# Performance work log

Hardware: AMD Instinct MI355X
Metric: run time of the kernel (lower is better)

## Reference

```python
import jax, jax.numpy as jnp
import numpy as np

D = 256
H = 4
HD = D // H


def rotate_half(x):
    xp = x.reshape(x.shape[:-1] + (-1, 2))
    x1, x2 = xp[..., 0], xp[..., 1]
    return jnp.stack((-x2, x1), axis=-1).reshape(x.shape)


def apply_rope(freqs, t):
    # freqs: [2, B, 1, N, HD]; t: [B, H, N, HD]
    return t * freqs[0] + rotate_half(t) * freqs[1]


def layernorm(x, g, b, eps=1e-5):
    m = jnp.mean(x, axis=-1, keepdims=True)
    v = jnp.var(x, axis=-1, keepdims=True)
    return (x - m) * jax.lax.rsqrt(v + eps) * g + b


def ffn(z, W1, b1, g, be, W2, b2):
    h = layernorm(z @ W1 + b1, g, be)
    h = jax.nn.gelu(h, approximate=False)
    return h @ W2 + b2


def heads_split(t):
    B, N, _ = t.shape
    return t.reshape(B, N, H, HD).transpose(0, 2, 1, 3)  # [B,H,N,HD]


def heads_merge(t):
    B, h, N, hd = t.shape
    return t.transpose(0, 2, 1, 3).reshape(B, N, h * hd)


def sdpa(q, k, v):
    s = q.shape[-1] ** (-0.5)
    sim = jnp.einsum('bhid,bhjd->bhij', q, k) * s
    attn = jax.nn.softmax(sim, axis=-1)
    return jnp.einsum('bhij,bhjd->bhid', attn, v)


def self_block(x, enc, Wqkv, bqkv, Wo, bo, W1, b1, g, be, W2, b2):
    B, N, _ = x.shape
    qkv = (x @ Wqkv + bqkv).reshape(B, N, H, HD, 3).transpose(0, 2, 1, 3, 4)
    q, k, v = qkv[..., 0], qkv[..., 1], qkv[..., 2]
    q = apply_rope(enc, q)
    k = apply_rope(enc, k)
    msg = heads_merge(sdpa(q, k, v)) @ Wo + bo
    return x + ffn(jnp.concatenate([x, msg], axis=-1), W1, b1, g, be, W2, b2)


def cross_block(x0, x1, Wqk, bqk, Wv, bv, Wo, bo, W1, b1, g, be, W2, b2):
    qk0 = heads_split(x0 @ Wqk + bqk)
    qk1 = heads_split(x1 @ Wqk + bqk)
    v0 = heads_split(x0 @ Wv + bv)
    v1 = heads_split(x1 @ Wv + bv)
    s = HD ** (-0.5)
    qk0 = qk0 * (s ** 0.5)
    qk1 = qk1 * (s ** 0.5)
    sim = jnp.einsum('bhid,bhjd->bhij', qk0, qk1)
    attn01 = jax.nn.softmax(sim, axis=-1)
    attn10 = jax.nn.softmax(sim.transpose(0, 1, 3, 2), axis=-1)
    m0 = jnp.einsum('bhij,bhjd->bhid', attn01, v1)
    m1 = jnp.einsum('bhij,bhjd->bhid', attn10, v0)
    m0 = heads_merge(m0) @ Wo + bo
    m1 = heads_merge(m1) @ Wo + bo
    x0 = x0 + ffn(jnp.concatenate([x0, m0], axis=-1), W1, b1, g, be, W2, b2)
    x1 = x1 + ffn(jnp.concatenate([x1, m1], axis=-1), W1, b1, g, be, W2, b2)
    return x0, x1


def setup_inputs() -> dict:
    key = jax.random.key(0)
    ks = jax.random.split(key, 24)
    B, N = 4, 2048
    desc0 = jax.random.normal(ks[0], (B, N, D), jnp.float32)
    desc1 = jax.random.normal(ks[1], (B, N, D), jnp.float32)
    encoding0 = jax.random.uniform(ks[2], (2, B, 1, N, HD), jnp.float32)
    encoding1 = jax.random.uniform(ks[3], (2, B, 1, N, HD), jnp.float32)

    def lin(k, fin, fout):
        k1, k2 = jax.random.split(k)
        W = jax.random.normal(k1, (fin, fout), jnp.float32) * (fin ** -0.5)
        b = jax.random.normal(k2, (fout,), jnp.float32) * 0.01
        return W, b

    Wqkv, bqkv = lin(ks[4], D, 3 * D)
    Wo_s, bo_s = lin(ks[5], D, D)
    W1_s, b1_s = lin(ks[6], 2 * D, 2 * D)
    g_s = jnp.ones((2 * D,), jnp.float32)
    be_s = jnp.zeros((2 * D,), jnp.float32)
    W2_s, b2_s = lin(ks[7], 2 * D, D)
    Wqk_c, bqk_c = lin(ks[8], D, D)
    Wv_c, bv_c = lin(ks[9], D, D)
    Wo_c, bo_c = lin(ks[10], D, D)
    W1_c, b1_c = lin(ks[11], 2 * D, 2 * D)
    g_c = jnp.ones((2 * D,), jnp.float32)
    be_c = jnp.zeros((2 * D,), jnp.float32)
    W2_c, b2_c = lin(ks[12], 2 * D, D)
    return dict(desc0=desc0, desc1=desc1, encoding0=encoding0, encoding1=encoding1,
                Wqkv=Wqkv, bqkv=bqkv, Wo_s=Wo_s, bo_s=bo_s,
                W1_s=W1_s, b1_s=b1_s, g_s=g_s, be_s=be_s, W2_s=W2_s, b2_s=b2_s,
                Wqk_c=Wqk_c, bqk_c=bqk_c, Wv_c=Wv_c, bv_c=bv_c, Wo_c=Wo_c, bo_c=bo_c,
                W1_c=W1_c, b1_c=b1_c, g_c=g_c, be_c=be_c, W2_c=W2_c, b2_c=b2_c)


def reference(desc0, desc1, encoding0, encoding1,
              Wqkv, bqkv, Wo_s, bo_s, W1_s, b1_s, g_s, be_s, W2_s, b2_s,
              Wqk_c, bqk_c, Wv_c, bv_c, Wo_c, bo_c, W1_c, b1_c, g_c, be_c, W2_c, b2_c):
    d0 = self_block(desc0, encoding0, Wqkv, bqkv, Wo_s, bo_s, W1_s, b1_s, g_s, be_s, W2_s, b2_s)
    d1 = self_block(desc1, encoding1, Wqkv, bqkv, Wo_s, bo_s, W1_s, b1_s, g_s, be_s, W2_s, b2_s)
    return cross_block(d0, d1, Wqk_c, bqk_c, Wv_c, bv_c, Wo_c, bo_c, W1_c, b1_c, g_c, be_c, W2_c, b2_c)
```

## Files before the change

### kernel.cpp

```cpp
#include <hip/hip_runtime.h>
#include <math.h>

#define BB 4
#define HH 4
#define NN 2048
#define DD 256
#define HDIM 64
#define NTOK 8192
#define NTOK2 16384

typedef __attribute__((ext_vector_type(8))) __bf16 bf16x8;
typedef __attribute__((ext_vector_type(8))) unsigned short ushort8;
typedef __attribute__((ext_vector_type(4))) float floatx4;
typedef __attribute__((ext_vector_type(4))) short short4v;

union U8 { ushort8 u; bf16x8 b; };
union U4 { unsigned int u[2]; unsigned long long l; short4v s; };

#define MFMA16(a, b, c) __builtin_amdgcn_mfma_f32_16x16x16bf16_1k(a, b, c, 0, 0, 0)

__device__ __forceinline__ unsigned short f2bf(float x) {
    unsigned int u = __float_as_uint(x);
    u += 0x7FFF + ((u >> 16) & 1);
    return (unsigned short)(u >> 16);
}
__device__ __forceinline__ float bf2f(unsigned short u) {
    return __uint_as_float(((unsigned int)u) << 16);
}
__device__ __forceinline__ unsigned int pkbf(float a, float b) {
    return ((__float_as_uint(a) + 0x8000u) >> 16) |
           ((__float_as_uint(b) + 0x8000u) & 0xFFFF0000u);
}

struct WTab {
    const float* w[7];
    unsigned short* o[7];
    int K[7];
    int N[7];
    int st[7];
    int t0[8];
};

__global__ __launch_bounds__(256) void wtrans(WTab tab)
{
    __shared__ float lds[32][33];
    const int t = threadIdx.x;
    int bid = blockIdx.x;
    int s = 0;
    while (bid >= tab.t0[s + 1]) s++;
    const int ti = bid - tab.t0[s];
    const int K = tab.K[s], N = tab.N[s], st = tab.st[s];
    const int tx = ti % (N / 32), ty = ti / (N / 32);
    const int k0 = ty * 32, n0 = tx * 32;
    const float* W = tab.w[s];
    unsigned short* Wt = tab.o[s];

    {
        int r = t >> 3, c = (t & 7) * 4;
        float4 a = *(const float4*)&W[(size_t)(k0 + r) * N + n0 + c];
        lds[r][c] = a.x; lds[r][c+1] = a.y; lds[r][c+2] = a.z; lds[r][c+3] = a.w;
    }
    __syncthreads();
    {
        int n = t >> 3, kq = (t & 7) * 4;
        ushort4 p;
        p.x = f2bf(lds[kq+0][n]); p.y = f2bf(lds[kq+1][n]);
        p.z = f2bf(lds[kq+2][n]); p.w = f2bf(lds[kq+3][n]);
        *(ushort4*)&Wt[(size_t)(n0 + n) * st + k0 + kq] = p;
    }
}

__global__ __launch_bounds__(256) void wfuse(
    const float* __restrict__ Wo_s, const float* __restrict__ W1_s,
    unsigned short* __restrict__ o_s,
    const float* __restrict__ Wo_c, const float* __restrict__ W1_c,
    unsigned short* __restrict__ o_c)
{
    __shared__ float wo[32][33];
    __shared__ float w1[32][68];
    const int t = threadIdx.x;
    const int bid = blockIdx.x;
    const int seg = bid >> 6, ti_ = bid & 63;
    const int i0 = (ti_ >> 3) * 32, n0 = (ti_ & 7) * 64;
    const float* Wo  = seg ? Wo_c : Wo_s;
    const float* W1b = (seg ? W1_c : W1_s) + 256 * 512;
    unsigned short* out = seg ? o_c : o_s;
    const int ti = t >> 3, tn = t & 7;

    float acc[8] = {};
    for (int jc = 0; jc < 256; jc += 32) {
        {
            int r = t >> 3, c = (t & 7) * 4;
            *(float4*)&wo[r][c] = *(const float4*)&Wo[(size_t)(i0 + r) * 256 + jc + c];
            int c8 = (t & 7) * 8;
            *(float4*)&w1[r][c8]     = *(const float4*)&W1b[(size_t)(jc + r) * 512 + n0 + c8];
            *(float4*)&w1[r][c8 + 4] = *(const float4*)&W1b[(size_t)(jc + r) * 512 + n0 + c8 + 4];
        }
        __syncthreads();
        #pragma unroll
        for (int j = 0; j < 32; j++) {
            float a = wo[ti][j];
            #pragma unroll
            for (int e = 0; e < 8; e++) acc[e] += a * w1[j][tn * 8 + e];
        }
        __syncthreads();
    }
    #pragma unroll
    for (int e = 0; e < 8; e++)
        out[(size_t)(n0 + tn * 8 + e) * 512 + 256 + i0 + ti] = f2bf(acc[e]);
}

__global__ __launch_bounds__(256) void bfuse(
    const float* bo_s, const float* W1_s, const float* b1_s, float* bs,
    const float* bo_c, const float* W1_c, const float* b1_c, float* bc)
{
    const int seg = blockIdx.x >> 1, half = blockIdx.x & 1;
    const int n = half * 256 + threadIdx.x;
    const float* bo  = seg ? bo_c : bo_s;
    const float* W1b = (seg ? W1_c : W1_s) + 256 * 512;
    const float* b1  = seg ? b1_c : b1_s;
    float* out       = seg ? bc : bs;
    float a = b1[n];
    for (int j = 0; j < 256; j++) a += bo[j] * W1b[(size_t)j * 512 + n];
    out[n] = a;
}

__global__ __launch_bounds__(256) void gemm_mfma(
    const unsigned short* __restrict__ A, int lda,
    const unsigned short* __restrict__ Wt, int K,
    const float* __restrict__ bias, const float* __restrict__ bias2, int mode,
    float* outF, unsigned short* outH0, unsigned short* outH1,
    unsigned short* outH2,
    int ldc, const float* R0, const float* R1)
{
    __shared__ __align__(16) unsigned short As[64 * 40];
    __shared__ __align__(16) unsigned short Bs[128 * 40];
    const int t = threadIdx.x;
    const int w = t >> 6, lane = t & 63, quad = lane >> 4, l15 = lane & 15;
    const int m0 = blockIdx.y * 64, n0 = blockIdx.x * 128;
    const int wn = w * 32;
    const int sar = t >> 2, sac = (t & 3) * 8;
    const int sbr = t >> 1, sbc = (t & 1) * 16;

    const unsigned short* Ap = A  + (size_t)(m0 + sar) * lda + sac;
    const unsigned short* Bp = Wt + (size_t)(n0 + sbr) * K   + sbc;

    ushort8 pa  = *(const ushort8*)(Ap);
    ushort8 pb0 = *(const ushort8*)(Bp);
    ushort8 pb1 = *(const ushort8*)(Bp + 8);

    floatx4 acc[4][2];
    #pragma unroll
    for (int i = 0; i < 4; i++)
        #pragma unroll
        for (int j = 0; j < 2; j++) acc[i][j] = (floatx4){0.f, 0.f, 0.f, 0.f};

    const int nk = K >> 5;
    for (int kk = 0; kk < nk; kk++) {
        *(ushort8*)&As[sar * 40 + sac]     = pa;
        *(ushort8*)&Bs[sbr * 40 + sbc]     = pb0;
        *(ushort8*)&Bs[sbr * 40 + sbc + 8] = pb1;
        __syncthreads();
        if (kk + 1 < nk) {
            int ko = (kk + 1) * 32;
            pa  = *(const ushort8*)(Ap + ko);
            pb0 = *(const ushort8*)(Bp + ko);
            pb1 = *(const ushort8*)(Bp + ko + 8);
        }
        U8 af[4], bf[2];
        #pragma unroll
        for (int i = 0; i < 4; i++)
            af[i].u = *(const ushort8*)&As[(i * 16 + l15) * 40 + quad * 8];
        #pragma unroll
        for (int j = 0; j < 2; j++)
            bf[j].u = *(const ushort8*)&Bs[(wn + j * 16 + l15) * 40 + quad * 8];
        #pragma unroll
        for (int i = 0; i < 4; i++)
            #pragma unroll
            for (int j = 0; j < 2; j++)
                acc[i][j] = __builtin_amdgcn_mfma_f32_16x16x32_bf16(af[i].b, bf[j].b, acc[i][j], 0, 0, 0);
        __syncthreads();
    }

    #pragma unroll
    for (int i = 0; i < 4; i++) {
        #pragma unroll
        for (int j = 0; j < 2; j++) {
            int col = n0 + wn + j * 16 + l15;
            float bv = (mode == 2 && col >= 256) ? bias2[col & 255] : bias[col];
            #pragma unroll
            for (int r = 0; r < 4; r++) {
                int grow = m0 + i * 16 + quad * 4 + r;
                float v = acc[i][j][r] + bv;
                if (mode == 1) {
                    outH0[(size_t)grow * ldc + col] = f2bf(v);
                } else if (mode == 2) {
                    int cc = col & 255;
                    int h = cc >> 6, d = cc & 63;
                    int ds = grow >> 13, b = (grow >> 11) & 3, n = grow & 2047;
                    int bh = ds * 16 + b * 4 + h;
                    if (col < 256)
                        outH0[((size_t)bh * NN + n) * HDIM + d] = f2bf(v);
                    else
                        outH1[((size_t)bh * HDIM + d) * NN + n] = f2bf(v);
                } else if (mode == 3) {
                    int sel = col % 3, cc = col / 3;
                    int h = cc >> 6, d = cc & 63;
                    int ds = grow >> 13, b = (grow >> 11) & 3, n = grow & 2047;
                    int bh = ds * 16 + b * 4 + h;
                    if (sel == 0)
                        outH0[((size_t)bh * NN + n) * HDIM + d] = f2bf(v);
                    else if (sel == 1)
                        outH1[((size_t)bh * NN + n) * HDIM + d] = f2bf(v);
                    else
                        outH2[((size_t)bh * HDIM + d) * NN + n] = f2bf(v);
                } else {
                    const float* R = (grow < NTOK) ? R0 : R1;
                    float vv = v + R[(size_t)(grow & 8191) * 256 + col];
                    outF[(size_t)grow * 256 + col] = vv;
                    if (outH0) outH0[(size_t)grow * 256 + col] = f2bf(vv);
                    if (outH1) outH1[(size_t)grow * 512 + col] = f2bf(vv);
                }
            }
        }
    }
}

__global__ __launch_bounds__(256) void rope_k(unsigned short* __restrict__ qb,
                                              unsigned short* __restrict__ kb,
                                              const float* __restrict__ enc0,
                                              const float* __restrict__ enc1)
{
    int i = blockIdx.x * 256 + threadIdx.x;
    int dp = (i & 31) * 2;
    int n  = (i >> 5) & (NN - 1);
    int h  = (i >> 16) & 3;
    int b  = (i >> 18) & 3;
    int ds = (i >> 20) & 1;
    int bf = (i >> 21) & 1;
    unsigned short* tq = (bf ? kb : qb) +
        (((size_t)(ds * 16 + b * 4 + h)) * NN + n) * HDIM + dp;
    const float* e0 = (ds ? enc1 : enc0) + ((size_t)b * NN + n) * HDIM + dp;
    const float* e1 = e0 + (size_t)BB * NN * HDIM;
    float x0 = bf2f(tq[0]), x1 = bf2f(tq[1]);
    float y0 = x0 * e0[0] - x1 * e1[0];
    float y1 = x1 * e0[1] + x0 * e1[1];
    tq[0] = f2bf(y0); tq[1] = f2bf(y1);
}

__global__ __launch_bounds__(256) void flash_attn(
    const unsigned short* __restrict__ Q, const unsigned short* __restrict__ K,
    const unsigned short* __restrict__ V, unsigned short* __restrict__ O,
    int ldo, int kvx, float qscale)
{
    __shared__ __align__(16) unsigned short Ks[64 * 72];
    __shared__ __align__(16) unsigned short Vt[64 * 72];

    const int t    = threadIdx.x;
    const int w    = t >> 6;
    const int lane = t & 63;
    const int quad = lane >> 4;
    const int l15  = lane & 15;
    const int bh   = blockIdx.y;
    const int kbh  = bh ^ kvx;
    const int q0   = blockIdx.x * 64;

    const unsigned short* Qb  = Q + (size_t)bh  * NN * HDIM;
    const unsigned short* Kb  = K + (size_t)kbh * NN * HDIM;
    const unsigned short* VTb = V + (size_t)kbh * NN * HDIM;

    const int srf = t >> 3, scf = (t & 7) * 8;

    const int qrow = q0 + w * 16 + l15;
    bf16x8 qf0, qf1;
    {
        U8 r0, r1, x0, x1;
        r0.u = *(const ushort8*)&Qb[(size_t)qrow * HDIM + quad * 8];
        r1.u = *(const ushort8*)&Qb[(size_t)qrow * HDIM + 32 + quad * 8];
        #pragma unroll
        for (int j = 0; j < 8; j++) {
            x0.u[j] = f2bf(bf2f(r0.u[j]) * qscale);
            x1.u[j] = f2bf(bf2f(r1.u[j]) * qscale);
        }
        qf0 = x0.b; qf1 = x1.b;
    }

    floatx4 o[4];
    #pragma unroll
    for (int c = 0; c < 4; c++) o[c] = (floatx4){0.f, 0.f, 0.f, 0.f};
    float m = -1e30f, l = 0.f;

    ushort8 ka0 = *(const ushort8*)&Kb[(size_t)srf * HDIM + scf];
    ushort8 ka1 = *(const ushort8*)&Kb[(size_t)(srf + 32) * HDIM + scf];
    ushort8 va0 = *(const ushort8*)&VTb[(size_t)srf * NN + scf];
    ushort8 va1 = *(const ushort8*)&VTb[(size_t)(srf + 32) * NN + scf];

    for (int j0 = 0; j0 < NN; j0 += 64) {
        *(ushort8*)&Ks[srf * 72 + scf]        = ka0;
        *(ushort8*)&Ks[(srf + 32) * 72 + scf] = ka1;
        *(ushort8*)&Vt[srf * 72 + scf]        = va0;
        *(ushort8*)&Vt[(srf + 32) * 72 + scf] = va1;
        __syncthreads();
        if (j0 + 64 < NN) {
            int jn = j0 + 64;
            ka0 = *(const ushort8*)&Kb[(size_t)(jn + srf) * HDIM + scf];
            ka1 = *(const ushort8*)&Kb[(size_t)(jn + srf + 32) * HDIM + scf];
            va0 = *(const ushort8*)&VTb[(size_t)srf * NN + jn + scf];
            va1 = *(const ushort8*)&VTb[(size_t)(srf + 32) * NN + jn + scf];
        }

        floatx4 s[4];
        #pragma unroll
        for (int t4 = 0; t4 < 4; t4++) {
            U8 k0, k1;
            k0.u = *(const ushort8*)&Ks[(t4 * 16 + l15) * 72 + quad * 8];
            k1.u = *(const ushort8*)&Ks[(t4 * 16 + l15) * 72 + 32 + quad * 8];
            floatx4 z = (floatx4){0.f, 0.f, 0.f, 0.f};
            z = __builtin_amdgcn_mfma_f32_16x16x32_bf16(k0.b, qf0, z, 0, 0, 0);
            z = __builtin_amdgcn_mfma_f32_16x16x32_bf16(k1.b, qf1, z, 0, 0, 0);
            s[t4] = z;
        }

        float mx = s[0][0];
        #pragma unroll
        for (int t4 = 0; t4 < 4; t4++)
            #pragma unroll
            for (int r = 0; r < 4; r++) mx = fmaxf(mx, s[t4][r]);
        mx = fmaxf(mx, __shfl_xor(mx, 16, 64));
        mx = fmaxf(mx, __shfl_xor(mx, 32, 64));
        float mn = fmaxf(m, mx);
        float al = exp2f(m - mn);
        m = mn;
        float rs = 0.f;
        #pragma unroll
        for (int t4 = 0; t4 < 4; t4++)
            #pragma unroll
            for (int r = 0; r < 4; r++) {
                float p = exp2f(s[t4][r] - mn);
                s[t4][r] = p;
                rs += p;
            }
        rs += __shfl_xor(rs, 16, 64);
        rs += __shfl_xor(rs, 32, 64);
        l = l * al + rs;
        #pragma unroll
        for (int c = 0; c < 4; c++)
            #pragma unroll
            for (int r = 0; r < 4; r++) o[c][r] *= al;

        short4v pf[4];
        #pragma unroll
        for (int t4 = 0; t4 < 4; t4++) {
            U4 pk;
            pk.u[0] = pkbf(s[t4][0], s[t4][1]);
            pk.u[1] = pkbf(s[t4][2], s[t4][3]);
            pf[t4] = pk.s;
        }

        #pragma unroll
        for (int c = 0; c < 4; c++) {
            #pragma unroll
            for (int t4 = 0; t4 < 4; t4++) {
                U4 vf;
                vf.l = *(const unsigned long long*)
                    &Vt[(c * 16 + l15) * 72 + t4 * 16 + quad * 4];
                o[c] = MFMA16(vf.s, pf[t4], o[c]);
            }
        }
        __syncthreads();
    }

    const int ds = bh >> 4, b = (bh >> 2) & 3, h = bh & 3;
    const int q = q0 + w * 16 + l15;
    const size_t row = (size_t)ds * NTOK + b * NN + q;
    float inv = 1.f / l;
    #pragma unroll
    for (int c = 0; c < 4; c++) {
        ushort4 pk;
        pk.x = f2bf(o[c][0] * inv);
        pk.y = f2bf(o[c][1] * inv);
        pk.z = f2bf(o[c][2] * inv);
        pk.w = f2bf(o[c][3] * inv);
        *(ushort4*)&O[row * ldo + h * HDIM + c * 16 + quad * 4] = pk;
    }
}

__global__ __launch_bounds__(256) void ln_gelu(
    unsigned short* __restrict__ hb, const float* __restrict__ g,
    const float* __restrict__ be)
{
    __shared__ float r1[4], r2[4];
    const int t = threadIdx.x;
    const size_t row = blockIdx.x;
    unsigned short* ip = hb + row * 512;
    float x0 = bf2f(ip[t]), x1 = bf2f(ip[t + 256]);
    float s = x0 + x1, ss = x0 * x0 + x1 * x1;
    #pragma unroll
    for (int o = 32; o > 0; o >>= 1) { s += __shfl_down(s, o); ss += __shfl_down(ss, o); }
    if ((t & 63) == 0) { r1[t >> 6] = s; r2[t >> 6] = ss; }
    __syncthreads();
    float S  = r1[0] + r1[1] + r1[2] + r1[3];
    float SS = r2[0] + r2[1] + r2[2] + r2[3];
    float mean = S * (1.f / 512.f);
    float var  = SS * (1.f / 512.f) - mean * mean;
    float inv  = rsqrtf(var + 1e-5f);
    float y0 = (x0 - mean) * inv * g[t]       + be[t];
    float y1 = (x1 - mean) * inv * g[t + 256] + be[t + 256];
    ip[t]       = f2bf(0.5f * y0 * (1.f + erff(y0 * 0.70710678f)));
    ip[t + 256] = f2bf(0.5f * y1 * (1.f + erff(y1 * 0.70710678f)));
}

__global__ __launch_bounds__(256) void copy_to_cat(
    const float* __restrict__ s0, const float* __restrict__ s1,
    unsigned short* __restrict__ cat)
{
    int i = blockIdx.x * 256 + threadIdx.x;
    int row = i >> 6, c4 = (i & 63) * 4;
    const float* s = (row < NTOK) ? s0 : s1;
    float4 a = *(const float4*)&s[(size_t)(row & 8191) * 256 + c4];
    ushort4 p = { f2bf(a.x), f2bf(a.y), f2bf(a.z), f2bf(a.w) };
    *(ushort4*)&cat[(size_t)row * 512 + c4] = p;
}

extern "C" void kernel_launch(void* const* d_in, const int* in_sizes, int n_in,
                              void* d_out, int out_size, void* d_ws, size_t ws_size,
                              hipStream_t stream)
{
    const float* desc0 = (const float*)d_in[0];
    const float* desc1 = (const float*)d_in[1];
    const float* enc0  = (const float*)d_in[2];
    const float* enc1  = (const float*)d_in[3];
    const float* Wqkv  = (const float*)d_in[4];  const float* bqkv  = (const float*)d_in[5];
    const float* Wo_s  = (const float*)d_in[6];  const float* bo_s  = (const float*)d_in[7];
    const float* W1_s  = (const float*)d_in[8];  const float* b1_s  = (const float*)d_in[9];
    const float* g_s   = (const float*)d_in[10]; const float* be_s  = (const float*)d_in[11];
    const float* W2_s  = (const float*)d_in[12]; const float* b2_s  = (const float*)d_in[13];
    const float* Wqk_c = (const float*)d_in[14]; const float* bqk_c = (const float*)d_in[15];
    const float* Wv_c  = (const float*)d_in[16]; const float* bv_c  = (const float*)d_in[17];
    const float* Wo_c  = (const float*)d_in[18]; const float* bo_c  = (const float*)d_in[19];
    const float* W1_c  = (const float*)d_in[20]; const float* b1_c  = (const float*)d_in[21];
    const float* g_c   = (const float*)d_in[22]; const float* be_c  = (const float*)d_in[23];
    const float* W2_c  = (const float*)d_in[24]; const float* b2_c  = (const float*)d_in[25];

    char* ws = (char*)d_ws;
    unsigned short* wt  = (unsigned short*)ws;
    unsigned short* qb  = (unsigned short*)(ws + 2490368);
    unsigned short* kb  = (unsigned short*)(ws + 10878976);
    unsigned short* vb  = (unsigned short*)(ws + 27656192);
    unsigned short* cat = (unsigned short*)(ws + 36044800);
    unsigned short* hb  = (unsigned short*)(ws + 52822016);
    unsigned short* dbf = (unsigned short*)(ws + 86376448);

    unsigned short* t_qkv  = wt;
    float*          bias_s = (float*)(wt + 196608);
    unsigned short* t_w1s  = wt + 262144;
    unsigned short* t_w2s  = wt + 524288;
    unsigned short* t_wqkc = wt + 655360;
    float*          bias_c = (float*)(wt + 786432);
    unsigned short* t_w1c  = wt + 851968;
    unsigned short* t_w2c  = wt + 1114112;

    float* outF = (float*)d_out;

    dim3 blk(256);

    WTab tab;
    tab.w[0] = Wqkv;  tab.o[0] = t_qkv;          tab.K[0] = 256; tab.N[0] = 768; tab.st[0] = 256;
    tab.w[1] = W1_s;  tab.o[1] = t_w1s;          tab.K[1] = 256; tab.N[1] = 512; tab.st[1] = 512;
    tab.w[2] = W2_s;  tab.o[2] = t_w2s;          tab.K[2] = 512; tab.N[2] = 256; tab.st[2] = 512;
    tab.w[3] = Wqk_c; tab.o[3] = t_wqkc;         tab.K[3] = 256; tab.N[3] = 256; tab.st[3] = 256;
    tab.w[4] = Wv_c;  tab.o[4] = t_wqkc + 65536; tab.K[4] = 256; tab.N[4] = 256; tab.st[4] = 256;
    tab.w[5] = W1_c;  tab.o[5] = t_w1c;          tab.K[5] = 256; tab.N[5] = 512; tab.st[5] = 512;
    tab.w[6] = W2_c;  tab.o[6] = t_w2c;          tab.K[6] = 512; tab.N[6] = 256; tab.st[6] = 512;
    int acc_t = 0;
    for (int s = 0; s < 7; s++) {
        tab.t0[s] = acc_t;
        acc_t += (tab.K[s] / 32) * (tab.N[s] / 32);
    }
    tab.t0[7] = acc_t;
    hipLaunchKernelGGL(wtrans, dim3(acc_t), blk, 0, stream, tab);
    hipLaunchKernelGGL(wfuse, dim3(128), blk, 0, stream,
                       Wo_s, W1_s, t_w1s, Wo_c, W1_c, t_w1c);
    hipLaunchKernelGGL(bfuse, dim3(4), blk, 0, stream,
                       bo_s, W1_s, b1_s, bias_s, bo_c, W1_c, b1_c, bias_c);

    auto gemm = [&](const unsigned short* A, int lda, const unsigned short* Wtp,
                    int K, const float* bias, const float* bias2, int Nc, int mode,
                    float* oF, unsigned short* oh0, unsigned short* oh1,
                    unsigned short* oh2, int ldc, const float* r0, const float* r1) {
        dim3 g(Nc / 128, NTOK2 / 64);
        hipLaunchKernelGGL(gemm_mfma, g, blk, 0, stream,
                           A, lda, Wtp, K, bias, bias2, mode,
                           oF, oh0, oh1, oh2, ldc, r0, r1);
    };

    const float QS = 0.125f * 1.44269504088896f;

    hipLaunchKernelGGL(copy_to_cat, dim3(4096), blk, 0, stream, desc0, desc1, cat);
    gemm(cat, 512, t_qkv, 256, bqkv, nullptr, 768, 3,
         nullptr, qb, kb, vb, 0, nullptr, nullptr);
    hipLaunchKernelGGL(rope_k, dim3(16384), blk, 0, stream, qb, kb, enc0, enc1);
    hipLaunchKernelGGL(flash_attn, dim3(NN / 64, 32), blk, 0, stream,
                       qb, kb, vb, cat + 256, 512, 0, QS);
    gemm(cat, 512, t_w1s, 512, bias_s, nullptr, 512, 1,
         nullptr, hb, nullptr, nullptr, 512, nullptr, nullptr);
    hipLaunchKernelGGL(ln_gelu, dim3(NTOK2), blk, 0, stream, hb, g_s, be_s);
    gemm(hb, 512, t_w2s, 512, b2_s, nullptr, 256, 4,
         outF, dbf, cat, nullptr, 256, desc0, desc1);

    gemm(dbf, 256, t_wqkc, 256, bqk_c, bv_c, 512, 2,
         nullptr, qb, vb, nullptr, 0, nullptr, nullptr);
    hipLaunchKernelGGL(flash_attn, dim3(NN / 64, 32), blk, 0, stream,
                       qb, qb, vb, cat + 256, 512, 16, QS);
    gemm(cat, 512, t_w1c, 512, bias_c, nullptr, 512, 1,
         nullptr, hb, nullptr, nullptr, 512, nullptr, nullptr);
    hipLaunchKernelGGL(ln_gelu, dim3(NTOK2), blk, 0, stream, hb, g_c, be_c);
    gemm(hb, 512, t_w2c, 512, b2_c, nullptr, 256, 4,
         outF, nullptr, nullptr, nullptr, 256, outF, outF + (size_t)NTOK * 256);
}
```

Measured before the change: 494.2 us.

## Enlarge GEMM tiles to 128x128, double flash-attention KV tile, skip redundant rescale

The projection GEMMs move to a 128x128 block tile with a 2x2 warp layout, so each warp computes a 64x64 sub-tile and operands get more reuse from shared memory. The W2 residual GEMM is split into its own specialized kernel that keeps the old 64x128 tile. Flash attention now stages 128 keys per iteration instead of 64, halving the number of barrier and softmax rounds. It also skips the running max/sum rescale when no lane's max increased. The larger tiles raise register and LDS use, which may lower occupancy, and the GEMMs launch fewer blocks.

```diff
diff --git a/kernel.cpp b/kernel.cpp
--- a/kernel.cpp
+++ b/kernel.cpp
@@ -125,59 +125,60 @@
     out[n] = a;
 }
 
-__global__ __launch_bounds__(256) void gemm_mfma(
+__global__ __launch_bounds__(256) void gemm128(
     const unsigned short* __restrict__ A, int lda,
     const unsigned short* __restrict__ Wt, int K,
     const float* __restrict__ bias, const float* __restrict__ bias2, int mode,
-    float* outF, unsigned short* outH0, unsigned short* outH1,
-    unsigned short* outH2,
-    int ldc, const float* R0, const float* R1)
-{
-    __shared__ __align__(16) unsigned short As[64 * 40];
+    unsigned short* outH0, unsigned short* outH1, unsigned short* outH2,
+    int ldc)
+{
+    __shared__ __align__(16) unsigned short As[128 * 40];
     __shared__ __align__(16) unsigned short Bs[128 * 40];
     const int t = threadIdx.x;
     const int w = t >> 6, lane = t & 63, quad = lane >> 4, l15 = lane & 15;
-    const int m0 = blockIdx.y * 64, n0 = blockIdx.x * 128;
-    const int wn = w * 32;
-    const int sar = t >> 2, sac = (t & 3) * 8;
-    const int sbr = t >> 1, sbc = (t & 1) * 16;
-
-    const unsigned short* Ap = A  + (size_t)(m0 + sar) * lda + sac;
-    const unsigned short* Bp = Wt + (size_t)(n0 + sbr) * K   + sbc;
-
-    ushort8 pa  = *(const ushort8*)(Ap);
+    const int m0 = blockIdx.y * 128, n0 = blockIdx.x * 128;
+    const int wm = (w >> 1) * 64, wn = (w & 1) * 64;
+    const int sr = t >> 1, sc = (t & 1) * 16;
+
+    const unsigned short* Ap = A  + (size_t)(m0 + sr) * lda + sc;
+    const unsigned short* Bp = Wt + (size_t)(n0 + sr) * K   + sc;
+
+    ushort8 pa0 = *(const ushort8*)(Ap);
+    ushort8 pa1 = *(const ushort8*)(Ap + 8);
     ushort8 pb0 = *(const ushort8*)(Bp);
     ushort8 pb1 = *(const ushort8*)(Bp + 8);
 
-    floatx4 acc[4][2];
+    floatx4 acc[4][4];
     #pragma unroll
     for (int i = 0; i < 4; i++)
         #pragma unroll
-        for (int j = 0; j < 2; j++) acc[i][j] = (floatx4){0.f, 0.f, 0.f, 0.f};
+        for (int j = 0; j < 4; j++) acc[i][j] = (floatx4){0.f, 0.f, 0.f, 0.f};
 
     const int nk = K >> 5;
     for (int kk = 0; kk < nk; kk++) {
-        *(ushort8*)&As[sar * 40 + sac]     = pa;
-        *(ushort8*)&Bs[sbr * 40 + sbc]     = pb0;
-        *(ushort8*)&Bs[sbr * 40 + sbc + 8] = pb1;
+        *(ushort8*)&As[sr * 40 + sc]     = pa0;
+        *(ushort8*)&As[sr * 40 + sc + 8] = pa1;
+        *(ushort8*)&Bs[sr * 40 + sc]     = pb0;
+        *(ushort8*)&Bs[sr * 40 + sc + 8] = pb1;
         __syncthreads();
         if (kk + 1 < nk) {
             int ko = (kk + 1) * 32;
-            pa  = *(const ushort8*)(Ap + ko);
+            pa0 = *(const ushort8*)(Ap + ko);
+            pa1 = *(const ushort8*)(Ap + ko + 8);
             pb0 = *(const ushort8*)(Bp + ko);
             pb1 = *(const ushort8*)(Bp + ko + 8);
         }
-        U8 af[4], bf[2];
+        U8 af[4], bf[4];
         #pragma unroll
         for (int i = 0; i < 4; i++)
-            af[i].u = *(const ushort8*)&As[(i * 16 + l15) * 40 + quad * 8];
-        #pragma unroll
-        for (int j = 0; j < 2; j++)
+            af[i].u = *(const ushort8*)&As[(wm + i * 16 + l15) * 40 + quad * 8];
+        #pragma unroll
+        for (int j = 0; j < 4; j++)
             bf[j].u = *(const ushort8*)&Bs[(wn + j * 16 + l15) * 40 + quad * 8];
         #pragma unroll
         for (int i = 0; i < 4; i++)
             #pragma unroll
-            for (int j = 0; j < 2; j++)
+            for (int j = 0; j < 4; j++)
                 acc[i][j] = __builtin_amdgcn_mfma_f32_16x16x32_bf16(af[i].b, bf[j].b, acc[i][j], 0, 0, 0);
         __syncthreads();
     }
@@ -185,12 +186,12 @@
     #pragma unroll
     for (int i = 0; i < 4; i++) {
         #pragma unroll
-        for (int j = 0; j < 2; j++) {
+        for (int j = 0; j < 4; j++) {
             int col = n0 + wn + j * 16 + l15;
             float bv = (mode == 2 && col >= 256) ? bias2[col & 255] : bias[col];
             #pragma unroll
             for (int r = 0; r < 4; r++) {
-                int grow = m0 + i * 16 + quad * 4 + r;
+                int grow = m0 + wm + i * 16 + quad * 4 + r;
                 float v = acc[i][j][r] + bv;
                 if (mode == 1) {
                     outH0[(size_t)grow * ldc + col] = f2bf(v);
@@ -203,7 +204,7 @@
                         outH0[((size_t)bh * NN + n) * HDIM + d] = f2bf(v);
                     else
                         outH1[((size_t)bh * HDIM + d) * NN + n] = f2bf(v);
-                } else if (mode == 3) {
+                } else {
                     int sel = col % 3, cc = col / 3;
                     int h = cc >> 6, d = cc & 63;
                     int ds = grow >> 13, b = (grow >> 11) & 3, n = grow & 2047;
@@ -214,13 +215,83 @@
                         outH1[((size_t)bh * NN + n) * HDIM + d] = f2bf(v);
                     else
                         outH2[((size_t)bh * HDIM + d) * NN + n] = f2bf(v);
-                } else {
-                    const float* R = (grow < NTOK) ? R0 : R1;
-                    float vv = v + R[(size_t)(grow & 8191) * 256 + col];
-                    outF[(size_t)grow * 256 + col] = vv;
-                    if (outH0) outH0[(size_t)grow * 256 + col] = f2bf(vv);
-                    if (outH1) outH1[(size_t)grow * 512 + col] = f2bf(vv);
                 }
+            }
+        }
+    }
+}
+
+__global__ __launch_bounds__(256) void gemm_w2(
+    const unsigned short* __restrict__ A,
+    const unsigned short* __restrict__ Wt,
+    const float* __restrict__ bias,
+    float* outF, unsigned short* outH0, unsigned short* outH1,
+    const float* R0, const float* R1)
+{
+    __shared__ __align__(16) unsigned short As[64 * 40];
+    __shared__ __align__(16) unsigned short Bs[128 * 40];
+    const int t = threadIdx.x;
+    const int w = t >> 6, lane = t & 63, quad = lane >> 4, l15 = lane & 15;
+    const int m0 = blockIdx.y * 64, n0 = blockIdx.x * 128;
+    const int wn = w * 32;
+    const int sar = t >> 2, sac = (t & 3) * 8;
+    const int sbr = t >> 1, sbc = (t & 1) * 16;
+    const int K = 512;
+
+    const unsigned short* Ap = A  + (size_t)(m0 + sar) * 512 + sac;
+    const unsigned short* Bp = Wt + (size_t)(n0 + sbr) * K   + sbc;
+
+    ushort8 pa  = *(const ushort8*)(Ap);
+    ushort8 pb0 = *(const ushort8*)(Bp);
+    ushort8 pb1 = *(const ushort8*)(Bp + 8);
+
+    floatx4 acc[4][2];
+    #pragma unroll
+    for (int i = 0; i < 4; i++)
+        #pragma unroll
+        for (int j = 0; j < 2; j++) acc[i][j] = (floatx4){0.f, 0.f, 0.f, 0.f};
+
+    const int nk = K >> 5;
+    for (int kk = 0; kk < nk; kk++) {
+        *(ushort8*)&As[sar * 40 + sac]     = pa;
+        *(ushort8*)&Bs[sbr * 40 + sbc]     = pb0;
+        *(ushort8*)&Bs[sbr * 40 + sbc + 8] = pb1;
+        __syncthreads();
+        if (kk + 1 < nk) {
+            int ko = (kk + 1) * 32;
+            pa  = *(const ushort8*)(Ap + ko);
+            pb0 = *(const ushort8*)(Bp + ko);
+            pb1 = *(const ushort8*)(Bp + ko + 8);
+        }
+        U8 af[4], bf[2];
+        #pragma unroll
+        for (int i = 0; i < 4; i++)
+            af[i].u = *(const ushort8*)&As[(i * 16 + l15) * 40 + quad * 8];
+        #pragma unroll
+        for (int j = 0; j < 2; j++)
+            bf[j].u = *(const ushort8*)&Bs[(wn + j * 16 + l15) * 40 + quad * 8];
+        #pragma unroll
+        for (int i = 0; i < 4; i++)
+            #pragma unroll
+            for (int j = 0; j < 2; j++)
+                acc[i][j] = __builtin_amdgcn_mfma_f32_16x16x32_bf16(af[i].b, bf[j].b, acc[i][j], 0, 0, 0);
+        __syncthreads();
+    }
+
+    #pragma unroll
+    for (int i = 0; i < 4; i++) {
+        #pragma unroll
+        for (int j = 0; j < 2; j++) {
+            int col = n0 + wn + j * 16 + l15;
+            float bv = bias[col];
+            #pragma unroll
+            for (int r = 0; r < 4; r++) {
+                int grow = m0 + i * 16 + quad * 4 + r;
+                const float* R = (grow < NTOK) ? R0 : R1;
+                float vv = acc[i][j][r] + bv + R[(size_t)(grow & 8191) * 256 + col];
+                outF[(size_t)grow * 256 + col] = vv;
+                if (outH0) outH0[(size_t)grow * 256 + col] = f2bf(vv);
+                if (outH1) outH1[(size_t)grow * 512 + col] = f2bf(vv);
             }
         }
     }
@@ -253,8 +324,8 @@
     const unsigned short* __restrict__ V, unsigned short* __restrict__ O,
     int ldo, int kvx, float qscale)
 {
-    __shared__ __align__(16) unsigned short Ks[64 * 72];
-    __shared__ __align__(16) unsigned short Vt[64 * 72];
+    __shared__ __align__(16) unsigned short Ks[128 * 72];
+    __shared__ __align__(16) unsigned short Vt[64 * 136];
 
     const int t    = threadIdx.x;
     const int w    = t >> 6;
@@ -269,7 +340,8 @@
     const unsigned short* Kb  = K + (size_t)kbh * NN * HDIM;
     const unsigned short* VTb = V + (size_t)kbh * NN * HDIM;
 
-    const int srf = t >> 3, scf = (t & 7) * 8;
+    const int krf = t >> 3, kcf = (t & 7) * 8;
+    const int vrf = t >> 4, vcf = (t & 15) * 8;
 
     const int qrow = q0 + w * 16 + l15;
     bf16x8 qf0, qf1;
@@ -290,81 +362,88 @@
     for (int c = 0; c < 4; c++) o[c] = (floatx4){0.f, 0.f, 0.f, 0.f};
     float m = -1e30f, l = 0.f;
 
-    ushort8 ka0 = *(const ushort8*)&Kb[(size_t)srf * HDIM + scf];
-    ushort8 ka1 = *(const ushort8*)&Kb[(size_t)(srf + 32) * HDIM + scf];
-    ushort8 va0 = *(const ushort8*)&VTb[(size_t)srf * NN + scf];
-    ushort8 va1 = *(const ushort8*)&VTb[(size_t)(srf + 32) * NN + scf];
-
-    for (int j0 = 0; j0 < NN; j0 += 64) {
-        *(ushort8*)&Ks[srf * 72 + scf]        = ka0;
-        *(ushort8*)&Ks[(srf + 32) * 72 + scf] = ka1;
-        *(ushort8*)&Vt[srf * 72 + scf]        = va0;
-        *(ushort8*)&Vt[(srf + 32) * 72 + scf] = va1;
-        __syncthreads();
-        if (j0 + 64 < NN) {
-            int jn = j0 + 64;
-            ka0 = *(const ushort8*)&Kb[(size_t)(jn + srf) * HDIM + scf];
-            ka1 = *(const ushort8*)&Kb[(size_t)(jn + srf + 32) * HDIM + scf];
-            va0 = *(const ushort8*)&VTb[(size_t)srf * NN + jn + scf];
-            va1 = *(const ushort8*)&VTb[(size_t)(srf + 32) * NN + jn + scf];
-        }
-
-        floatx4 s[4];
-        #pragma unroll
-        for (int t4 = 0; t4 < 4; t4++) {
+    ushort8 ka[4], va[4];
+    #pragma unroll
+    for (int i = 0; i < 4; i++) {
+        ka[i] = *(const ushort8*)&Kb[(size_t)(krf + 32 * i) * HDIM + kcf];
+        va[i] = *(const ushort8*)&VTb[(size_t)(vrf + 16 * i) * NN + vcf];
+    }
+
+    for (int j0 = 0; j0 < NN; j0 += 128) {
+        #pragma unroll
+        for (int i = 0; i < 4; i++) {
+            *(ushort8*)&Ks[(krf + 32 * i) * 72 + kcf]  = ka[i];
+            *(ushort8*)&Vt[(vrf + 16 * i) * 136 + vcf] = va[i];
+        }
+        __syncthreads();
+        if (j0 + 128 < NN) {
+            int jn = j0 + 128;
+            #pragma unroll
+            for (int i = 0; i < 4; i++) {
+                ka[i] = *(const ushort8*)&Kb[(size_t)(jn + krf + 32 * i) * HDIM + kcf];
+                va[i] = *(const ushort8*)&VTb[(size_t)(vrf + 16 * i) * NN + jn + vcf];
+            }
+        }
+
+        floatx4 s[8];
+        #pragma unroll
+        for (int t8 = 0; t8 < 8; t8++) {
             U8 k0, k1;
-            k0.u = *(const ushort8*)&Ks[(t4 * 16 + l15) * 72 + quad * 8];
-            k1.u = *(const ushort8*)&Ks[(t4 * 16 + l15) * 72 + 32 + quad * 8];
+            k0.u = *(const ushort8*)&Ks[(t8 * 16 + l15) * 72 + quad * 8];
+            k1.u = *(const ushort8*)&Ks[(t8 * 16 + l15) * 72 + 32 + quad * 8];
             floatx4 z = (floatx4){0.f, 0.f, 0.f, 0.f};
             z = __builtin_amdgcn_mfma_f32_16x16x32_bf16(k0.b, qf0, z, 0, 0, 0);
             z = __builtin_amdgcn_mfma_f32_16x16x32_bf16(k1.b, qf1, z, 0, 0, 0);
-            s[t4] = z;
+            s[t8] = z;
         }
 
         float mx = s[0][0];
         #pragma unroll
-        for (int t4 = 0; t4 < 4; t4++)
-            #pragma unroll
-            for (int r = 0; r < 4; r++) mx = fmaxf(mx, s[t4][r]);
+        for (int t8 = 0; t8 < 8; t8++)
+            #pragma unroll
+            for (int r = 0; r < 4; r++) mx = fmaxf(mx, s[t8][r]);
         mx = fmaxf(mx, __shfl_xor(mx, 16, 64));
         mx = fmaxf(mx, __shfl_xor(mx, 32, 64));
-        float mn = fmaxf(m, mx);
-        float al = exp2f(m - mn);
-        m = mn;
+        if (__ballot(mx > m)) {
+            float mn = fmaxf(m, mx);
+            float al = exp2f(m - mn);
+            m = mn;
+            l *= al;
+            #pragma unroll
+            for (int c = 0; c < 4; c++)
+                #pragma unroll
+                for (int r = 0; r < 4; r++) o[c][r] *= al;
+        }
         float rs = 0.f;
         #pragma unroll
-        for (int t4 = 0; t4 < 4; t4++)
+        for (int t8 = 0; t8 < 8; t8++)
             #pragma unroll
             for (int r = 0; r < 4; r++) {
-                float p = exp2f(s[t4][r] - mn);
-                s[t4][r] = p;
+                float p = exp2f(s[t8][r] - m);
+                s[t8][r] = p;
                 rs += p;
             }
         rs += __shfl_xor(rs, 16, 64);
         rs += __shfl_xor(rs, 32, 64);
-        l = l * al + rs;
-        #pragma unroll
-        for (int c = 0; c < 4; c++)
-            #pragma unroll
-            for (int r = 0; r < 4; r++) o[c][r] *= al;
-
-        short4v pf[4];
-        #pragma unroll
-        for (int t4 = 0; t4 < 4; t4++) {
+        l += rs;
+
+        short4v pf[8];
+        #pragma unroll
+        for (int t8 = 0; t8 < 8; t8++) {
             U4 pk;
-            pk.u[0] = pkbf(s[t4][0], s[t4][1]);
-            pk.u[1] = pkbf(s[t4][2], s[t4][3]);
-            pf[t4] = pk.s;
+            pk.u[0] = pkbf(s[t8][0], s[t8][1]);
+            pk.u[1] = pkbf(s[t8][2], s[t8][3]);
+            pf[t8] = pk.s;
         }
 
         #pragma unroll
         for (int c = 0; c < 4; c++) {
             #pragma unroll
-            for (int t4 = 0; t4 < 4; t4++) {
+            for (int t8 = 0; t8 < 8; t8++) {
                 U4 vf;
                 vf.l = *(const unsigned long long*)
-                    &Vt[(c * 16 + l15) * 72 + t4 * 16 + quad * 4];
-                o[c] = MFMA16(vf.s, pf[t4], o[c]);
+                    &Vt[(c * 16 + l15) * 136 + t8 * 16 + quad * 4];
+                o[c] = MFMA16(vf.s, pf[t8], o[c]);
             }
         }
         __syncthreads();
@@ -484,37 +563,33 @@
     hipLaunchKernelGGL(bfuse, dim3(4), blk, 0, stream,
                        bo_s, W1_s, b1_s, bias_s, bo_c, W1_c, b1_c, bias_c);
 
-    auto gemm = [&](const unsigned short* A, int lda, const unsigned short* Wtp,
+    auto g128 = [&](const unsigned short* A, int lda, const unsigned short* Wtp,
                     int K, const float* bias, const float* bias2, int Nc, int mode,
-                    float* oF, unsigned short* oh0, unsigned short* oh1,
-                    unsigned short* oh2, int ldc, const float* r0, const float* r1) {
-        dim3 g(Nc / 128, NTOK2 / 64);
-        hipLaunchKernelGGL(gemm_mfma, g, blk, 0, stream,
-                           A, lda, Wtp, K, bias, bias2, mode,
-                           oF, oh0, oh1, oh2, ldc, r0, r1);
+                    unsigned short* oh0, unsigned short* oh1, unsigned short* oh2,
+                    int ldc) {
+        dim3 g(Nc / 128, NTOK2 / 128);
+        hipLaunchKernelGGL(gemm128, g, blk, 0, stream,
+                           A, lda, Wtp, K, bias, bias2, mode, oh0, oh1, oh2, ldc);
     };
 
     const float QS = 0.125f * 1.44269504088896f;
 
     hipLaunchKernelGGL(copy_to_cat, dim3(4096), blk, 0, stream, desc0, desc1, cat);
-    gemm(cat, 512, t_qkv, 256, bqkv, nullptr, 768, 3,
-         nullptr, qb, kb, vb, 0, nullptr, nullptr);
+    g128(cat, 512, t_qkv, 256, bqkv, nullptr, 768, 3, qb, kb, vb, 0);
     hipLaunchKernelGGL(rope_k, dim3(16384), blk, 0, stream, qb, kb, enc0, enc1);
     hipLaunchKernelGGL(flash_attn, dim3(NN / 64, 32), blk, 0, stream,
                        qb, kb, vb, cat + 256, 512, 0, QS);
-    gemm(cat, 512, t_w1s, 512, bias_s, nullptr, 512, 1,
-         nullptr, hb, nullptr, nullptr, 512, nullptr, nullptr);
+    g128(cat, 512, t_w1s, 512, bias_s, nullptr, 512, 1, hb, nullptr, nullptr, 512);
     hipLaunchKernelGGL(ln_gelu, dim3(NTOK2), blk, 0, stream, hb, g_s, be_s);
-    gemm(hb, 512, t_w2s, 512, b2_s, nullptr, 256, 4,
-         outF, dbf, cat, nullptr, 256, desc0, desc1);
-
-    gemm(dbf, 256, t_wqkc, 256, bqk_c, bv_c, 512, 2,
-         nullptr, qb, vb, nullptr, 0, nullptr, nullptr);
+    hipLaunchKernelGGL(gemm_w2, dim3(2, 256), blk, 0, stream,
+                       hb, t_w2s, b2_s, outF, dbf, cat, desc0, desc1);
+
+    g128(dbf, 256, t_wqkc, 256, bqk_c, bv_c, 512, 2, qb, vb, nullptr, 0);
     hipLaunchKernelGGL(flash_attn, dim3(NN / 64, 32), blk, 0, stream,
                        qb, qb, vb, cat + 256, 512, 16, QS);
-    gemm(cat, 512, t_w1c, 512, bias_c, nullptr, 512, 1,
-         nullptr, hb, nullptr, nullptr, 512, nullptr, nullptr);
+    g128(cat, 512, t_w1c, 512, bias_c, nullptr, 512, 1, hb, nullptr, nullptr, 512);
     hipLaunchKernelGGL(ln_gelu, dim3(NTOK2), blk, 0, stream, hb, g_c, be_c);
-    gemm(hb, 512, t_w2c, 512, b2_c, nullptr, 256, 4,
-         outF, nullptr, nullptr, nullptr, 256, outF, outF + (size_t)NTOK * 256);
-}
+    hipLaunchKernelGGL(gemm_w2, dim3(2, 256), blk, 0, stream,
+                       hb, t_w2c, b2_c, outF, nullptr, nullptr,
+                       outF, outF + (size_t)NTOK * 256);
+}
```

New measurement: 497.6 us. Within noise of the previous version (+0.7%).

## Fuse input cast into QKV GEMM and Q-rope plus desc copy into attention

Applied to the files above, without the earlier changes.

The QKV GEMM now reads the fp32 descriptors directly and converts them to bf16 while loading, so the separate copy_to_cat kernel is removed. The flash attention kernel applies RoPE to Q in registers when it loads Q. It also writes the bf16 copy of the descriptors into the left half of the concat buffer. The rope kernel now only processes K, halving its launch. This removes launches and round trips through global memory, at the cost of a runtime branch in the GEMM A-load and extra strided fp32 encoding reads in attention.

```diff
diff --git a/kernel.cpp b/kernel.cpp
--- a/kernel.cpp
+++ b/kernel.cpp
@@ -126,7 +126,7 @@
 }
 
 __global__ __launch_bounds__(256) void gemm_mfma(
-    const unsigned short* __restrict__ A, int lda,
+    const void* A0v, const void* A1v, int lda, int a_f32,
     const unsigned short* __restrict__ Wt, int K,
     const float* __restrict__ bias, const float* __restrict__ bias2, int mode,
     float* outF, unsigned short* outH0, unsigned short* outH1,
@@ -141,11 +141,26 @@
     const int wn = w * 32;
     const int sar = t >> 2, sac = (t & 3) * 8;
     const int sbr = t >> 1, sbc = (t & 1) * 16;
-
-    const unsigned short* Ap = A  + (size_t)(m0 + sar) * lda + sac;
-    const unsigned short* Bp = Wt + (size_t)(n0 + sbr) * K   + sbc;
-
-    ushort8 pa  = *(const ushort8*)(Ap);
+    const int mside = (m0 >= 8192) ? 1 : 0;
+    const int mrow = m0 & 8191;
+    const unsigned short* Ah = (const unsigned short*)(mside ? A1v : A0v);
+    const float* Af = (const float*)(mside ? A1v : A0v);
+
+    const unsigned short* Bp = Wt + (size_t)(n0 + sbr) * K + sbc;
+
+    auto loadA = [&](int ko) -> ushort8 {
+        if (a_f32) {
+            float4 x = *(const float4*)&Af[(size_t)(mrow + sar) * lda + ko + sac];
+            float4 y = *(const float4*)&Af[(size_t)(mrow + sar) * lda + ko + sac + 4];
+            ushort8 r;
+            r[0] = f2bf(x.x); r[1] = f2bf(x.y); r[2] = f2bf(x.z); r[3] = f2bf(x.w);
+            r[4] = f2bf(y.x); r[5] = f2bf(y.y); r[6] = f2bf(y.z); r[7] = f2bf(y.w);
+            return r;
+        }
+        return *(const ushort8*)&Ah[(size_t)(mrow + sar) * lda + ko + sac];
+    };
+
+    ushort8 pa  = loadA(0);
     ushort8 pb0 = *(const ushort8*)(Bp);
     ushort8 pb1 = *(const ushort8*)(Bp + 8);
 
@@ -163,7 +178,7 @@
         __syncthreads();
         if (kk + 1 < nk) {
             int ko = (kk + 1) * 32;
-            pa  = *(const ushort8*)(Ap + ko);
+            pa  = loadA(ko);
             pb0 = *(const ushort8*)(Bp + ko);
             pb1 = *(const ushort8*)(Bp + ko + 8);
         }
@@ -226,8 +241,7 @@
     }
 }
 
-__global__ __launch_bounds__(256) void rope_k(unsigned short* __restrict__ qb,
-                                              unsigned short* __restrict__ kb,
+__global__ __launch_bounds__(256) void rope_k(unsigned short* __restrict__ kb,
                                               const float* __restrict__ enc0,
                                               const float* __restrict__ enc1)
 {
@@ -237,8 +251,7 @@
     int h  = (i >> 16) & 3;
     int b  = (i >> 18) & 3;
     int ds = (i >> 20) & 1;
-    int bf = (i >> 21) & 1;
-    unsigned short* tq = (bf ? kb : qb) +
+    unsigned short* tq = kb +
         (((size_t)(ds * 16 + b * 4 + h)) * NN + n) * HDIM + dp;
     const float* e0 = (ds ? enc1 : enc0) + ((size_t)b * NN + n) * HDIM + dp;
     const float* e1 = e0 + (size_t)BB * NN * HDIM;
@@ -251,7 +264,9 @@
 __global__ __launch_bounds__(256) void flash_attn(
     const unsigned short* __restrict__ Q, const unsigned short* __restrict__ K,
     const unsigned short* __restrict__ V, unsigned short* __restrict__ O,
-    int ldo, int kvx, float qscale)
+    int ldo, int kvx, float qscale,
+    const float* __restrict__ e0g, const float* __restrict__ e1g,
+    const float* __restrict__ d0, const float* __restrict__ d1)
 {
     __shared__ __align__(16) unsigned short Ks[64 * 72];
     __shared__ __align__(16) unsigned short Vt[64 * 72];
@@ -264,6 +279,7 @@
     const int bh   = blockIdx.y;
     const int kbh  = bh ^ kvx;
     const int q0   = blockIdx.x * 64;
+    const int ds   = bh >> 4, b = (bh >> 2) & 3, h = bh & 3;
 
     const unsigned short* Qb  = Q + (size_t)bh  * NN * HDIM;
     const unsigned short* Kb  = K + (size_t)kbh * NN * HDIM;
@@ -277,10 +293,31 @@
         U8 r0, r1, x0, x1;
         r0.u = *(const ushort8*)&Qb[(size_t)qrow * HDIM + quad * 8];
         r1.u = *(const ushort8*)&Qb[(size_t)qrow * HDIM + 32 + quad * 8];
+        float xa[8], xb[8];
+        #pragma unroll
+        for (int j = 0; j < 8; j++) { xa[j] = bf2f(r0.u[j]); xb[j] = bf2f(r1.u[j]); }
+        if (e0g) {
+            const float* eb = ds ? e1g : e0g;
+            size_t base = ((size_t)(b * NN + qrow)) * HDIM;
+            const float* f0a = eb + base + quad * 8;
+            const float* f1a = f0a + (size_t)BB * NN * HDIM;
+            const float* f0b = eb + base + 32 + quad * 8;
+            const float* f1b = f0b + (size_t)BB * NN * HDIM;
+            float ya[8], yb[8];
+            #pragma unroll
+            for (int p = 0; p < 4; p++) {
+                ya[2*p]   = xa[2*p]   * f0a[2*p]   - xa[2*p+1] * f1a[2*p];
+                ya[2*p+1] = xa[2*p+1] * f0a[2*p+1] + xa[2*p]   * f1a[2*p+1];
+                yb[2*p]   = xb[2*p]   * f0b[2*p]   - xb[2*p+1] * f1b[2*p];
+                yb[2*p+1] = xb[2*p+1] * f0b[2*p+1] + xb[2*p]   * f1b[2*p+1];
+            }
+            #pragma unroll
+            for (int j = 0; j < 8; j++) { xa[j] = ya[j]; xb[j] = yb[j]; }
+        }
         #pragma unroll
         for (int j = 0; j < 8; j++) {
-            x0.u[j] = f2bf(bf2f(r0.u[j]) * qscale);
-            x1.u[j] = f2bf(bf2f(r1.u[j]) * qscale);
+            x0.u[j] = f2bf(xa[j] * qscale);
+            x1.u[j] = f2bf(xb[j] * qscale);
         }
         qf0 = x0.b; qf1 = x1.b;
     }
@@ -370,7 +407,6 @@
         __syncthreads();
     }
 
-    const int ds = bh >> 4, b = (bh >> 2) & 3, h = bh & 3;
     const int q = q0 + w * 16 + l15;
     const size_t row = (size_t)ds * NTOK + b * NN + q;
     float inv = 1.f / l;
@@ -382,6 +418,16 @@
         pk.z = f2bf(o[c][2] * inv);
         pk.w = f2bf(o[c][3] * inv);
         *(ushort4*)&O[row * ldo + h * HDIM + c * 16 + quad * 4] = pk;
+    }
+    if (d0) {
+        const float* dsc = ds ? d1 : d0;
+        #pragma unroll
+        for (int c = 0; c < 4; c++) {
+            float4 a = *(const float4*)
+                &dsc[((size_t)(b * NN + q)) * 256 + h * HDIM + c * 16 + quad * 4];
+            ushort4 pk = { f2bf(a.x), f2bf(a.y), f2bf(a.z), f2bf(a.w) };
+            *(ushort4*)&O[row * ldo + h * HDIM + c * 16 + quad * 4 - 256] = pk;
+        }
     }
 }
 
@@ -410,18 +456,6 @@
     ip[t + 256] = f2bf(0.5f * y1 * (1.f + erff(y1 * 0.70710678f)));
 }
 
-__global__ __launch_bounds__(256) void copy_to_cat(
-    const float* __restrict__ s0, const float* __restrict__ s1,
-    unsigned short* __restrict__ cat)
-{
-    int i = blockIdx.x * 256 + threadIdx.x;
-    int row = i >> 6, c4 = (i & 63) * 4;
-    const float* s = (row < NTOK) ? s0 : s1;
-    float4 a = *(const float4*)&s[(size_t)(row & 8191) * 256 + c4];
-    ushort4 p = { f2bf(a.x), f2bf(a.y), f2bf(a.z), f2bf(a.w) };
-    *(ushort4*)&cat[(size_t)row * 512 + c4] = p;
-}
-
 extern "C" void kernel_launch(void* const* d_in, const int* in_sizes, int n_in,
                               void* d_out, int out_size, void* d_ws, size_t ws_size,
                               hipStream_t stream)
@@ -484,37 +518,39 @@
     hipLaunchKernelGGL(bfuse, dim3(4), blk, 0, stream,
                        bo_s, W1_s, b1_s, bias_s, bo_c, W1_c, b1_c, bias_c);
 
-    auto gemm = [&](const unsigned short* A, int lda, const unsigned short* Wtp,
-                    int K, const float* bias, const float* bias2, int Nc, int mode,
+    auto gemm = [&](const void* A0, const void* A1, int lda, int a_f32,
+                    const unsigned short* Wtp, int K, const float* bias,
+                    const float* bias2, int Nc, int mode,
                     float* oF, unsigned short* oh0, unsigned short* oh1,
                     unsigned short* oh2, int ldc, const float* r0, const float* r1) {
         dim3 g(Nc / 128, NTOK2 / 64);
         hipLaunchKernelGGL(gemm_mfma, g, blk, 0, stream,
-                           A, lda, Wtp, K, bias, bias2, mode,
+                           A0, A1, lda, a_f32, Wtp, K, bias, bias2, mode,
                            oF, oh0, oh1, oh2, ldc, r0, r1);
     };
 
     const float QS = 0.125f * 1.44269504088896f;
 
-    hipLaunchKernelGGL(copy_to_cat, dim3(4096), blk, 0, stream, desc0, desc1, cat);
-    gemm(cat, 512, t_qkv, 256, bqkv, nullptr, 768, 3,
+    gemm(desc0, desc1, 256, 1, t_qkv, 256, bqkv, nullptr, 768, 3,
          nullptr, qb, kb, vb, 0, nullptr, nullptr);
-    hipLaunchKernelGGL(rope_k, dim3(16384), blk, 0, stream, qb, kb, enc0, enc1);
+    hipLaunchKernelGGL(rope_k, dim3(8192), blk, 0, stream, kb, enc0, enc1);
     hipLaunchKernelGGL(flash_attn, dim3(NN / 64, 32), blk, 0, stream,
-                       qb, kb, vb, cat + 256, 512, 0, QS);
-    gemm(cat, 512, t_w1s, 512, bias_s, nullptr, 512, 1,
+                       qb, kb, vb, cat + 256, 512, 0, QS,
+                       enc0, enc1, desc0, desc1);
+    gemm(cat, cat + (size_t)8192 * 512, 512, 0, t_w1s, 512, bias_s, nullptr, 512, 1,
          nullptr, hb, nullptr, nullptr, 512, nullptr, nullptr);
     hipLaunchKernelGGL(ln_gelu, dim3(NTOK2), blk, 0, stream, hb, g_s, be_s);
-    gemm(hb, 512, t_w2s, 512, b2_s, nullptr, 256, 4,
+    gemm(hb, hb + (size_t)8192 * 512, 512, 0, t_w2s, 512, b2_s, nullptr, 256, 4,
          outF, dbf, cat, nullptr, 256, desc0, desc1);
 
-    gemm(dbf, 256, t_wqkc, 256, bqk_c, bv_c, 512, 2,
+    gemm(dbf, dbf + (size_t)8192 * 256, 256, 0, t_wqkc, 256, bqk_c, bv_c, 512, 2,
          nullptr, qb, vb, nullptr, 0, nullptr, nullptr);
     hipLaunchKernelGGL(flash_attn, dim3(NN / 64, 32), blk, 0, stream,
-                       qb, qb, vb, cat + 256, 512, 16, QS);
-    gemm(cat, 512, t_w1c, 512, bias_c, nullptr, 512, 1,
+                       qb, qb, vb, cat + 256, 512, 16, QS,
+                       nullptr, nullptr, nullptr, nullptr);
+    gemm(cat, cat + (size_t)8192 * 512, 512, 0, t_w1c, 512, bias_c, nullptr, 512, 1,
          nullptr, hb, nullptr, nullptr, 512, nullptr, nullptr);
     hipLaunchKernelGGL(ln_gelu, dim3(NTOK2), blk, 0, stream, hb, g_c, be_c);
-    gemm(hb, 512, t_w2c, 512, b2_c, nullptr, 256, 4,
+    gemm(hb, hb + (size_t)8192 * 512, 512, 0, t_w2c, 512, b2_c, nullptr, 256, 4,
          outF, nullptr, nullptr, nullptr, 256, outF, outF + (size_t)NTOK * 256);
 }
```

Result: no change. 496.3 us (+0.4%).
